# Kernel optimization log

Measured on AMD Instinct MI355X. Metric: run time of the kernel, lower is better.

Reference implementation:

```python
import jax, jax.numpy as jnp
import numpy as np

N_DIM = 512
HEADS = 8
NUM_EXPERTS = 65536
NUM_KEYS = 256      # sqrt(NUM_EXPERTS)
DIM_KEY = 256       # N_DIM // 2
TOPK = 16           # num_experts_per_head (also product_key_topk)
SCALE = 0.02


def setup_inputs() -> dict:
    key = jax.random.key(0)
    k0, k1, k2, k3, k4 = jax.random.split(key, 5)
    x = jax.random.normal(k0, (1, 2048, N_DIM), dtype=jnp.float32)
    W_q = jax.random.normal(k1, (N_DIM, 2 * HEADS * DIM_KEY), dtype=jnp.float32) * SCALE
    keys = jax.random.normal(k2, (HEADS, NUM_KEYS, 2, DIM_KEY), dtype=jnp.float32) * SCALE
    down_embed = jax.random.normal(k3, (NUM_EXPERTS, N_DIM), dtype=jnp.float32) * SCALE
    up_embed = jax.random.normal(k4, (NUM_EXPERTS, N_DIM), dtype=jnp.float32) * SCALE
    return {"x": x, "W_q": W_q, "keys": keys, "down_embed": down_embed, "up_embed": up_embed}


def reference(x, W_q, keys, down_embed, up_embed):
    b, n, d = x.shape
    # queries: [b,n,2*h*dk] -> [2,b,n,h,dk]
    q = (x @ W_q).reshape(b, n, 2, HEADS, DIM_KEY).transpose(2, 0, 1, 3, 4)
    # similarity against product keys: [2,b,n,h,num_keys]
    sim = jnp.einsum('pbnhd,hkpd->pbnhk', q, keys)
    sx, ix = jax.lax.top_k(sim[0], TOPK)   # [b,n,h,TOPK]
    sy, iy = jax.lax.top_k(sim[1], TOPK)
    # cartesian product of the two top-k sets -> [b,n,h,TOPK*TOPK]
    all_scores = (sx[..., :, None] + sy[..., None, :]).reshape(b, n, HEADS, TOPK * TOPK)
    scores, pk_idx = jax.lax.top_k(all_scores, TOPK)  # [b,n,h,TOPK]
    # NOTE: original module indexes embeddings with pk_idx (flat top-k positions),
    # reproduced faithfully here.
    w_down = down_embed[pk_idx]  # [b,n,h,TOPK,d]
    w_up = up_embed[pk_idx]      # [b,n,h,TOPK,d]
    h = jnp.einsum('bnd,bnhkd->bnhk', x, w_down)
    h = jax.nn.gelu(h, approximate=False)
    h = jax.nn.softmax(scores, axis=-1) * h
    return jnp.einsum('bnhk,bnhkd->bnd', h, w_up)
```

## Files before the change

kernel.cpp:

```cpp
#include <hip/hip_runtime.h>
#include <math.h>

#define N_TOK 2048
#define NDIM 512
#define HEADS 8
#define TOPK 16
#define QCOLS 4096

typedef __attribute__((ext_vector_type(8))) _Float16 f16x8;
typedef __attribute__((ext_vector_type(4))) float f32x4;

__device__ __forceinline__ unsigned short f32_to_f16(float f) {
    _Float16 h = (_Float16)f;
    return __builtin_bit_cast(unsigned short, h);
}
__device__ __forceinline__ float f16_to_f32(unsigned short u) {
    return (float)__builtin_bit_cast(_Float16, u);
}
__device__ __forceinline__ void gl_lds16(const void* g, void* l) {
    __builtin_amdgcn_global_load_lds(
        (const __attribute__((address_space(1))) void*)g,
        (__attribute__((address_space(3))) void*)l, 16, 0, 0);
}

__device__ __forceinline__ void split_f4(const float* __restrict__ src,
                                         unsigned short* __restrict__ dh,
                                         unsigned short* __restrict__ dl,
                                         int i) {
    float4 v = reinterpret_cast<const float4*>(src)[i];
    float vv[4] = {v.x, v.y, v.z, v.w};
    ushort4 h, lo;
    unsigned short* hp = &h.x; unsigned short* lp = &lo.x;
    #pragma unroll
    for (int q = 0; q < 4; ++q) {
        unsigned short hh = f32_to_f16(vv[q]);
        hp[q] = hh;
        lp[q] = f32_to_f16(vv[q] - f16_to_f32(hh));
    }
    reinterpret_cast<ushort4*>(dh)[i] = h;
    reinterpret_cast<ushort4*>(dl)[i] = lo;
}

__global__ __launch_bounds__(256) void kP_split(const float* __restrict__ x,
                                                const float* __restrict__ Wq,
                                                const float* __restrict__ keys,
                                                const float* __restrict__ down,
                                                const float* __restrict__ up,
                                                unsigned short* __restrict__ xh,
                                                unsigned short* __restrict__ xl,
                                                unsigned short* __restrict__ Wqh,
                                                unsigned short* __restrict__ Wql,
                                                unsigned short* __restrict__ ksh,
                                                unsigned short* __restrict__ ksl,
                                                unsigned short* __restrict__ Mth,
                                                unsigned short* __restrict__ Mtl,
                                                unsigned short* __restrict__ upTh,
                                                unsigned short* __restrict__ upTl) {
    const int bid = blockIdx.x;
    const int tid = threadIdx.x;
    if (bid < 256) {
        #pragma unroll
        for (int t = 0; t < 4; ++t) split_f4(x, xh, xl, bid * 1024 + t * 256 + tid);
        return;
    }
    if (bid < 768) {
        const int b = bid - 256;
        #pragma unroll
        for (int t = 0; t < 4; ++t) split_f4(Wq, Wqh, Wql, b * 1024 + t * 256 + tid);
        return;
    }
    if (bid < 1024) {
        const int b = bid - 768;
        #pragma unroll
        for (int t = 0; t < 4; ++t) split_f4(keys, ksh, ksl, b * 1024 + t * 256 + tid);
        return;
    }
    if (bid < 1280) {
        const int e = bid - 1024;
        const int d0 = tid * 2;
        float2 v = *reinterpret_cast<const float2*>(&down[(size_t)e * NDIM + d0]);
        ushort2 h, lo;
        unsigned short h0 = f32_to_f16(v.x);
        unsigned short h1 = f32_to_f16(v.y);
        h.x = h0; h.y = h1;
        lo.x = f32_to_f16(v.x - f16_to_f32(h0));
        lo.y = f32_to_f16(v.y - f16_to_f32(h1));
        *reinterpret_cast<ushort2*>(&Mth[(size_t)(QCOLS + e) * NDIM + d0]) = h;
        *reinterpret_cast<ushort2*>(&Mtl[(size_t)(QCOLS + e) * NDIM + d0]) = lo;
        return;
    }
    const int b = bid - 1280;
    #pragma unroll
    for (int dd = 0; dd < 8; ++dd) {
        const int d = b * 8 + dd;
        const int e = tid;
        const float v = up[(size_t)e * NDIM + d];
        unsigned short hh = f32_to_f16(v);
        upTh[(size_t)d * 256 + e] = hh;
        upTl[(size_t)d * 256 + e] = f32_to_f16(v - f16_to_f32(hh));
    }
}

__global__ __launch_bounds__(256) void kQ_m1(const unsigned short* __restrict__ Wqh,
                                             const unsigned short* __restrict__ Wql,
                                             const unsigned short* __restrict__ ksh,
                                             const unsigned short* __restrict__ ksl,
                                             unsigned short* __restrict__ Mth,
                                             unsigned short* __restrict__ Mtl) {
    __shared__ __align__(16) char lds[36864];
    const int tid = threadIdx.x;
    const int w = tid >> 6, l = tid & 63;
    const int c0 = blockIdx.x * 32;
    const int ph = blockIdx.y;
    const int p = ph >> 3, h = ph & 7;
    const int off = p * 2048 + h * 256;
    f32x4 acc[2][4] = {};

    for (int s = 0; s < 8; ++s) {
        const int kk = s * 32;
        __syncthreads();
        {
            const int q = w * 1024 + l * 16;
            const int r = q >> 7;
            const int bsw = (q & 127) ^ ((r & 7) << 4);
            const unsigned short* src = (bsw < 64)
                ? Wqh + (size_t)(c0 + r) * QCOLS + off + kk + (bsw >> 1)
                : Wql + (size_t)(c0 + r) * QCOLS + off + kk + ((bsw - 64) >> 1);
            gl_lds16(src, lds + w * 1024);
        }
        #pragma unroll
        for (int t = 0; t < 8; ++t) {
            const int q = w * 8192 + t * 1024 + l * 16;
            const int r = q >> 7;
            const int bsw = (q & 127) ^ ((r & 7) << 4);
            const unsigned short* src = (bsw < 64)
                ? ksh + ((size_t)(h * 256 + r) * 2 + p) * 256 + kk + (bsw >> 1)
                : ksl + ((size_t)(h * 256 + r) * 2 + p) * 256 + kk + ((bsw - 64) >> 1);
            gl_lds16(src, lds + 4096 + w * 8192 + t * 1024);
        }
        __syncthreads();
        const int bq = (l >> 4) * 16;
        f16x8 ah[2], al[2];
        #pragma unroll
        for (int mi = 0; mi < 2; ++mi) {
            const int ra = mi * 16 + (l & 15);
            const int swz = (ra & 7) << 4;
            ah[mi] = *(const f16x8*)(lds + ra * 128 + (bq ^ swz));
            al[mi] = *(const f16x8*)(lds + ra * 128 + ((bq + 64) ^ swz));
        }
        __builtin_amdgcn_s_setprio(1);
        #pragma unroll
        for (int nj = 0; nj < 4; ++nj) {
            const int rb = w * 64 + nj * 16 + (l & 15);
            const int swz = (rb & 7) << 4;
            f16x8 bh = *(const f16x8*)(lds + 4096 + rb * 128 + (bq ^ swz));
            f16x8 bl = *(const f16x8*)(lds + 4096 + rb * 128 + ((bq + 64) ^ swz));
            #pragma unroll
            for (int mi = 0; mi < 2; ++mi) {
                acc[mi][nj] = __builtin_amdgcn_mfma_f32_16x16x32_f16(ah[mi], bh, acc[mi][nj], 0, 0, 0);
                acc[mi][nj] = __builtin_amdgcn_mfma_f32_16x16x32_f16(ah[mi], bl, acc[mi][nj], 0, 0, 0);
                acc[mi][nj] = __builtin_amdgcn_mfma_f32_16x16x32_f16(al[mi], bh, acc[mi][nj], 0, 0, 0);
            }
        }
        __builtin_amdgcn_s_setprio(0);
    }
    #pragma unroll
    for (int mi = 0; mi < 2; ++mi)
        #pragma unroll
        for (int nj = 0; nj < 4; ++nj) {
            const int k = w * 64 + nj * 16 + (l & 15);
            const int cb = c0 + mi * 16 + (l >> 4) * 4;
            ushort4 h4, l4;
            unsigned short* hp = &h4.x; unsigned short* lp = &l4.x;
            #pragma unroll
            for (int r = 0; r < 4; ++r) {
                const float v = acc[mi][nj][r];
                unsigned short hh = f32_to_f16(v);
                hp[r] = hh;
                lp[r] = f32_to_f16(v - f16_to_f32(hh));
            }
            *reinterpret_cast<ushort4*>(&Mth[(size_t)(off + k) * NDIM + cb]) = h4;
            *reinterpret_cast<ushort4*>(&Mtl[(size_t)(off + k) * NDIM + cb]) = l4;
        }
}

#define BM 64
#define BN 256
#define BK 32
__global__ __launch_bounds__(256, 3) void kF_gemm(const unsigned short* __restrict__ xh,
                                                  const unsigned short* __restrict__ xl,
                                                  const unsigned short* __restrict__ Mth,
                                                  const unsigned short* __restrict__ Mtl,
                                                  float* __restrict__ T,
                                                  float* __restrict__ D) {
    __shared__ __align__(16) char lds[40960];
    const int tid = threadIdx.x;
    const int w = tid >> 6, l = tid & 63;
    const int row0 = blockIdx.x * BM;
    const int g = blockIdx.y;
    const int colbase = g * 256;
    f32x4 acc[4][4] = {};

    for (int s = 0; s < 16; ++s) {
        const int kk = s * BK;
        __syncthreads();
        #pragma unroll
        for (int t = 0; t < 2; ++t) {
            const int q = w * 2048 + t * 1024 + l * 16;
            const int r = q >> 7;
            const int bsw = (q & 127) ^ ((r & 7) << 4);
            const unsigned short* src = (bsw < 64)
                ? xh + (size_t)(row0 + r) * NDIM + kk + (bsw >> 1)
                : xl + (size_t)(row0 + r) * NDIM + kk + ((bsw - 64) >> 1);
            gl_lds16(src, lds + w * 2048 + t * 1024);
        }
        #pragma unroll
        for (int t = 0; t < 8; ++t) {
            const int q = w * 8192 + t * 1024 + l * 16;
            const int r = q >> 7;
            const int bsw = (q & 127) ^ ((r & 7) << 4);
            const unsigned short* src = (bsw < 64)
                ? Mth + (size_t)(colbase + r) * NDIM + kk + (bsw >> 1)
                : Mtl + (size_t)(colbase + r) * NDIM + kk + ((bsw - 64) >> 1);
            gl_lds16(src, lds + 8192 + w * 8192 + t * 1024);
        }
        __syncthreads();
        const int bq = (l >> 4) * 16;
        f16x8 ah[4], al[4];
        #pragma unroll
        for (int mi = 0; mi < 4; ++mi) {
            const int ra = mi * 16 + (l & 15);
            const int swz = (ra & 7) << 4;
            ah[mi] = *(const f16x8*)(lds + ra * 128 + (bq ^ swz));
            al[mi] = *(const f16x8*)(lds + ra * 128 + ((bq + 64) ^ swz));
        }
        __builtin_amdgcn_s_setprio(1);
        #pragma unroll
        for (int nj = 0; nj < 4; ++nj) {
            const int rb = w * 64 + nj * 16 + (l & 15);
            const int swz = (rb & 7) << 4;
            f16x8 bh = *(const f16x8*)(lds + 8192 + rb * 128 + (bq ^ swz));
            f16x8 bl = *(const f16x8*)(lds + 8192 + rb * 128 + ((bq + 64) ^ swz));
            #pragma unroll
            for (int mi = 0; mi < 4; ++mi) {
                acc[mi][nj] = __builtin_amdgcn_mfma_f32_16x16x32_f16(ah[mi], bh, acc[mi][nj], 0, 0, 0);
                acc[mi][nj] = __builtin_amdgcn_mfma_f32_16x16x32_f16(ah[mi], bl, acc[mi][nj], 0, 0, 0);
                acc[mi][nj] = __builtin_amdgcn_mfma_f32_16x16x32_f16(al[mi], bh, acc[mi][nj], 0, 0, 0);
            }
        }
        __builtin_amdgcn_s_setprio(0);
    }
    __syncthreads();

    if (g == 16) {
        #pragma unroll
        for (int mi = 0; mi < 4; ++mi)
            #pragma unroll
            for (int nj = 0; nj < 4; ++nj)
                #pragma unroll
                for (int r = 0; r < 4; ++r) {
                    const int row = row0 + mi * 16 + (l >> 4) * 4 + r;
                    const int col = w * 64 + nj * 16 + (l & 15);
                    D[(size_t)row * 256 + col] = acc[mi][nj][r];
                }
        return;
    }

    float* Cl = (float*)lds;
    const int grp = tid >> 4;
    const int lam = tid & 15;
    for (int c = 0; c < 4; ++c) {
        #pragma unroll
        for (int nj = 0; nj < 4; ++nj)
            #pragma unroll
            for (int r = 0; r < 4; ++r)
                Cl[((l >> 4) * 4 + r) * 260 + w * 64 + nj * 16 + (l & 15)] = acc[c][nj][r];
        __syncthreads();
        float v[16];
        #pragma unroll
        for (int j = 0; j < 16; ++j) v[j] = Cl[grp * 260 + lam + 16 * j];
        #pragma unroll
        for (int k = 2; k <= 16; k <<= 1)
            #pragma unroll
            for (int j = k >> 1; j > 0; j >>= 1)
                #pragma unroll
                for (int i = 0; i < 16; ++i) {
                    const int l2 = i ^ j;
                    if (l2 > i) {
                        const bool asc = ((i & k) == 0);
                        const float lo = fminf(v[i], v[l2]), hi = fmaxf(v[i], v[l2]);
                        v[i] = asc ? lo : hi;
                        v[l2] = asc ? hi : lo;
                    }
                }
        #pragma unroll
        for (int lvl = 1; lvl <= 8; lvl <<= 1) {
            float m[16];
            #pragma unroll
            for (int q = 0; q < 16; ++q)
                m[q] = fmaxf(v[q], __shfl_xor(v[15 - q], lvl));
            #pragma unroll
            for (int j = 8; j > 0; j >>= 1)
                #pragma unroll
                for (int i = 0; i < 16; ++i) {
                    const int l2 = i ^ j;
                    if (l2 > i) {
                        const float lo = fminf(m[i], m[l2]), hi = fmaxf(m[i], m[l2]);
                        m[i] = lo; m[l2] = hi;
                    }
                }
            #pragma unroll
            for (int q = 0; q < 16; ++q) v[q] = m[q];
        }
        const int n = row0 + c * 16 + grp;
        T[((size_t)n * 16 + g) * 16 + lam] = v[15 - lam];
        __syncthreads();
    }
}

__device__ const unsigned short CAND_TBL[32] = {
    0x0100, 0x0302, 0x0504, 0x0706, 0x0908, 0x0B0A, 0x0D0C, 0x0F0E,
    0x1110, 0x1312, 0x1514, 0x1716,
    0x2120, 0x2322, 0x3024, 0x3231, 0x4033, 0x4241,
    0x5150, 0x6160, 0x7170,
    0x9080, 0xB0A0, 0xD0C0, 0xF0E0,
    0xFFFF, 0xFFFF, 0xFFFF, 0xFFFF, 0xFFFF, 0xFFFF, 0xFFFF
};

__device__ __forceinline__ float sel16(const float a[16], int i) {
    float b0 = (i & 1) ? a[1] : a[0];
    float b1 = (i & 1) ? a[3] : a[2];
    float b2 = (i & 1) ? a[5] : a[4];
    float b3 = (i & 1) ? a[7] : a[6];
    float b4 = (i & 1) ? a[9] : a[8];
    float b5 = (i & 1) ? a[11] : a[10];
    float b6 = (i & 1) ? a[13] : a[12];
    float b7 = (i & 1) ? a[15] : a[14];
    float c0 = (i & 2) ? b1 : b0;
    float c1 = (i & 2) ? b3 : b2;
    float c2 = (i & 2) ? b5 : b4;
    float c3 = (i & 2) ? b7 : b6;
    float d0 = (i & 4) ? c1 : c0;
    float d1 = (i & 4) ? c3 : c2;
    return (i & 8) ? d1 : d0;
}

__global__ __launch_bounds__(256) void kC_combine(const float* __restrict__ T,
                                                  const float* __restrict__ D,
                                                  unsigned short* __restrict__ Wh,
                                                  unsigned short* __restrict__ Wl) {
    __shared__ unsigned long long ckey[8][50];
    __shared__ float winval[8][16];
    __shared__ int winflat[8][16];
    __shared__ int Wrow[256];

    const int tid = threadIdx.x;
    const int n = blockIdx.x;
    const int h = tid >> 5;
    const int lam = tid & 15;

    Wrow[tid] = 0;

    float sxd[16], syd[16];
    const float* t0 = &T[((size_t)n * 16 + h) * 16];
    const float* t1 = &T[((size_t)n * 16 + 8 + h) * 16];
    #pragma unroll
    for (int q = 0; q < 16; ++q) { sxd[q] = t0[q]; syd[q] = t1[q]; }

    const int lc = tid & 31;
    const unsigned int cw = CAND_TBL[lc];
    unsigned long long mykey[2]; float myval[2]; int myflat[2]; int myrank[2] = {0, 0};
    #pragma unroll
    for (int u = 0; u < 2; ++u) {
        const int fl = (cw >> (8 * u)) & 0xFF;
        const float sv = sel16(sxd, fl >> 4) + sel16(syd, fl & 15);
        const unsigned int uv = __float_as_uint(sv);
        const unsigned int mo = (uv & 0x80000000u) ? ~uv : (uv | 0x80000000u);
        mykey[u] = ((unsigned long long)mo << 8) | (unsigned long long)(255 - fl);
        myval[u] = sv; myflat[u] = fl;
        const int slot = lc * 2 + u;
        if (slot < 50) ckey[h][slot] = mykey[u];
    }
    __syncthreads();
    for (int kk = 0; kk < 50; ++kk) {
        const unsigned long long ok = ckey[h][kk];
        myrank[0] += (ok > mykey[0]) ? 1 : 0;
        myrank[1] += (ok > mykey[1]) ? 1 : 0;
    }
    #pragma unroll
    for (int u = 0; u < 2; ++u)
        if (myrank[u] < 16) { winval[h][myrank[u]] = myval[u]; winflat[h][myrank[u]] = myflat[u]; }
    __syncthreads();

    if (!(tid & 16)) {
        const float sc = winval[h][lam];
        const float m0 = winval[h][0];
        float e = expf(sc - m0);
        float esum = e;
        #pragma unroll
        for (int off = 1; off < 16; off <<= 1) esum += __shfl_xor(esum, off);
        const int fl = winflat[h][lam];
        const float hv = D[(size_t)n * 256 + fl];
        const float gg = 0.5f * hv * (1.0f + erff(hv * 0.70710678118654752f));
        const float wv = (e / esum) * gg;
        atomicAdd(&Wrow[fl], __float2int_rn(wv * 4194304.0f));
    }
    __syncthreads();
    const float wfin = (float)Wrow[tid] * (1.0f / 4194304.0f);
    const unsigned short hh = f32_to_f16(wfin);
    Wh[(size_t)n * 256 + tid] = hh;
    Wl[(size_t)n * 256 + tid] = f32_to_f16(wfin - f16_to_f32(hh));
}

__global__ __launch_bounds__(256) void k5_mfma(const unsigned short* __restrict__ Wh,
                                               const unsigned short* __restrict__ Wl,
                                               const unsigned short* __restrict__ upTh,
                                               const unsigned short* __restrict__ upTl,
                                               float* __restrict__ out) {
    __shared__ __align__(16) char lds[20480];
    const int tid = threadIdx.x;
    const int w = tid >> 6, l = tid & 63;
    const int n0 = blockIdx.x * 32;
    const int d0 = blockIdx.y * 128;
    f32x4 acc[2][2] = {};

    for (int s = 0; s < 8; ++s) {
        const int kk = s * 32;
        __syncthreads();
        {
            const int q = w * 1024 + l * 16;
            const int r = q >> 7;
            const int bsw = (q & 127) ^ ((r & 7) << 4);
            const unsigned short* src = (bsw < 64)
                ? Wh + (size_t)(n0 + r) * 256 + kk + (bsw >> 1)
                : Wl + (size_t)(n0 + r) * 256 + kk + ((bsw - 64) >> 1);
            gl_lds16(src, lds + w * 1024);
        }
        #pragma unroll
        for (int t = 0; t < 4; ++t) {
            const int q = w * 4096 + t * 1024 + l * 16;
            const int r = q >> 7;
            const int bsw = (q & 127) ^ ((r & 7) << 4);
            const unsigned short* src = (bsw < 64)
                ? upTh + (size_t)(d0 + r) * 256 + kk + (bsw >> 1)
                : upTl + (size_t)(d0 + r) * 256 + kk + ((bsw - 64) >> 1);
            gl_lds16(src, lds + 4096 + w * 4096 + t * 1024);
        }
        __syncthreads();
        const int bq = (l >> 4) * 16;
        f16x8 ah[2], al[2];
        #pragma unroll
        for (int mi = 0; mi < 2; ++mi) {
            const int ra = mi * 16 + (l & 15);
            const int swz = (ra & 7) << 4;
            ah[mi] = *(const f16x8*)(lds + ra * 128 + (bq ^ swz));
            al[mi] = *(const f16x8*)(lds + ra * 128 + ((bq + 64) ^ swz));
        }
        #pragma unroll
        for (int nj = 0; nj < 2; ++nj) {
            const int rb = w * 32 + nj * 16 + (l & 15);
            const int swz = (rb & 7) << 4;
            f16x8 bh = *(const f16x8*)(lds + 4096 + rb * 128 + (bq ^ swz));
            f16x8 bl = *(const f16x8*)(lds + 4096 + rb * 128 + ((bq + 64) ^ swz));
            #pragma unroll
            for (int mi = 0; mi < 2; ++mi) {
                acc[mi][nj] = __builtin_amdgcn_mfma_f32_16x16x32_f16(ah[mi], bh, acc[mi][nj], 0, 0, 0);
                acc[mi][nj] = __builtin_amdgcn_mfma_f32_16x16x32_f16(ah[mi], bl, acc[mi][nj], 0, 0, 0);
                acc[mi][nj] = __builtin_amdgcn_mfma_f32_16x16x32_f16(al[mi], bh, acc[mi][nj], 0, 0, 0);
            }
        }
    }
    #pragma unroll
    for (int mi = 0; mi < 2; ++mi)
        #pragma unroll
        for (int nj = 0; nj < 2; ++nj)
            #pragma unroll
            for (int r = 0; r < 4; ++r) {
                const int row = n0 + mi * 16 + (l >> 4) * 4 + r;
                const int col = d0 + w * 32 + nj * 16 + (l & 15);
                out[(size_t)row * NDIM + col] = acc[mi][nj][r];
            }
}

extern "C" void kernel_launch(void* const* d_in, const int* in_sizes, int n_in,
                              void* d_out, int out_size, void* d_ws, size_t ws_size,
                              hipStream_t stream) {
    const float* x    = (const float*)d_in[0];
    const float* Wq   = (const float*)d_in[1];
    const float* keys = (const float*)d_in[2];
    const float* down = (const float*)d_in[3];
    const float* up   = (const float*)d_in[4];
    float* out = (float*)d_out;

    char* ws = (char*)d_ws;
    unsigned short* Mth  = (unsigned short*)(ws);
    unsigned short* Mtl  = (unsigned short*)(ws + 4456448);
    unsigned short* xh   = (unsigned short*)(ws + 8912896);
    unsigned short* xl   = (unsigned short*)(ws + 11010048);
    unsigned short* Wqh  = (unsigned short*)(ws + 13107200);
    unsigned short* Wql  = (unsigned short*)(ws + 17301504);
    unsigned short* ksh  = (unsigned short*)(ws + 21495808);
    unsigned short* ksl  = (unsigned short*)(ws + 23592960);
    unsigned short* upTh = (unsigned short*)(ws + 25690112);
    unsigned short* upTl = (unsigned short*)(ws + 25952256);
    float* T             = (float*)(ws + 26214400);
    float* D             = (float*)(ws + 28311552);
    unsigned short* Wh   = (unsigned short*)(ws + 30408704);
    unsigned short* Wl   = (unsigned short*)(ws + 31457280);

    kP_split<<<1344, 256, 0, stream>>>(x, Wq, keys, down, up,
                                       xh, xl, Wqh, Wql, ksh, ksl, Mth, Mtl, upTh, upTl);
    kQ_m1<<<dim3(16, 16), 256, 0, stream>>>(Wqh, Wql, ksh, ksl, Mth, Mtl);
    kF_gemm<<<dim3(32, 17), 256, 0, stream>>>(xh, xl, Mth, Mtl, T, D);
    kC_combine<<<2048, 256, 0, stream>>>(T, D, Wh, Wl);
    k5_mfma<<<dim3(64, 4), 256, 0, stream>>>(Wh, Wl, upTh, upTl, out);
}
```

Measured before the change: 94.20 us.

## Enlarge fused GEMM tile to 256x256 with 1024 threads and scale split low parts

Result: slower. 353.4 us (+275.2%).

```diff
diff --git a/kernel.cpp b/kernel.cpp
--- a/kernel.cpp
+++ b/kernel.cpp
@@ -6,6 +6,8 @@
 #define HEADS 8
 #define TOPK 16
 #define QCOLS 4096
+#define LSC 4096.0f
+#define ILSC (1.0f/4096.0f)
 
 typedef __attribute__((ext_vector_type(8))) _Float16 f16x8;
 typedef __attribute__((ext_vector_type(4))) float f32x4;
@@ -23,10 +25,10 @@
         (__attribute__((address_space(3))) void*)l, 16, 0, 0);
 }
 
-__device__ __forceinline__ void split_f4(const float* __restrict__ src,
-                                         unsigned short* __restrict__ dh,
-                                         unsigned short* __restrict__ dl,
-                                         int i) {
+__device__ __forceinline__ void split_f4s(const float* __restrict__ src,
+                                          unsigned short* __restrict__ dh,
+                                          unsigned short* __restrict__ dl,
+                                          int i, float lsc) {
     float4 v = reinterpret_cast<const float4*>(src)[i];
     float vv[4] = {v.x, v.y, v.z, v.w};
     ushort4 h, lo;
@@ -35,7 +37,7 @@
     for (int q = 0; q < 4; ++q) {
         unsigned short hh = f32_to_f16(vv[q]);
         hp[q] = hh;
-        lp[q] = f32_to_f16(vv[q] - f16_to_f32(hh));
+        lp[q] = f32_to_f16((vv[q] - f16_to_f32(hh)) * lsc);
     }
     reinterpret_cast<ushort4*>(dh)[i] = h;
     reinterpret_cast<ushort4*>(dl)[i] = lo;
@@ -60,19 +62,19 @@
     const int tid = threadIdx.x;
     if (bid < 256) {
         #pragma unroll
-        for (int t = 0; t < 4; ++t) split_f4(x, xh, xl, bid * 1024 + t * 256 + tid);
+        for (int t = 0; t < 4; ++t) split_f4s(x, xh, xl, bid * 1024 + t * 256 + tid, 1.0f);
         return;
     }
     if (bid < 768) {
         const int b = bid - 256;
         #pragma unroll
-        for (int t = 0; t < 4; ++t) split_f4(Wq, Wqh, Wql, b * 1024 + t * 256 + tid);
+        for (int t = 0; t < 4; ++t) split_f4s(Wq, Wqh, Wql, b * 1024 + t * 256 + tid, LSC);
         return;
     }
     if (bid < 1024) {
         const int b = bid - 768;
         #pragma unroll
-        for (int t = 0; t < 4; ++t) split_f4(keys, ksh, ksl, b * 1024 + t * 256 + tid);
+        for (int t = 0; t < 4; ++t) split_f4s(keys, ksh, ksl, b * 1024 + t * 256 + tid, LSC);
         return;
     }
     if (bid < 1280) {
@@ -97,7 +99,7 @@
         const float v = up[(size_t)e * NDIM + d];
         unsigned short hh = f32_to_f16(v);
         upTh[(size_t)d * 256 + e] = hh;
-        upTl[(size_t)d * 256 + e] = f32_to_f16(v - f16_to_f32(hh));
+        upTl[(size_t)d * 256 + e] = f32_to_f16((v - f16_to_f32(hh)) * LSC);
     }
 }
 
@@ -114,7 +116,8 @@
     const int ph = blockIdx.y;
     const int p = ph >> 3, h = ph & 7;
     const int off = p * 2048 + h * 256;
-    f32x4 acc[2][4] = {};
+    f32x4 acch[2][4] = {};
+    f32x4 accl[2][4] = {};
 
     for (int s = 0; s < 8; ++s) {
         const int kk = s * 32;
@@ -157,9 +160,9 @@
             f16x8 bl = *(const f16x8*)(lds + 4096 + rb * 128 + ((bq + 64) ^ swz));
             #pragma unroll
             for (int mi = 0; mi < 2; ++mi) {
-                acc[mi][nj] = __builtin_amdgcn_mfma_f32_16x16x32_f16(ah[mi], bh, acc[mi][nj], 0, 0, 0);
-                acc[mi][nj] = __builtin_amdgcn_mfma_f32_16x16x32_f16(ah[mi], bl, acc[mi][nj], 0, 0, 0);
-                acc[mi][nj] = __builtin_amdgcn_mfma_f32_16x16x32_f16(al[mi], bh, acc[mi][nj], 0, 0, 0);
+                acch[mi][nj] = __builtin_amdgcn_mfma_f32_16x16x32_f16(ah[mi], bh, acch[mi][nj], 0, 0, 0);
+                accl[mi][nj] = __builtin_amdgcn_mfma_f32_16x16x32_f16(ah[mi], bl, accl[mi][nj], 0, 0, 0);
+                accl[mi][nj] = __builtin_amdgcn_mfma_f32_16x16x32_f16(al[mi], bh, accl[mi][nj], 0, 0, 0);
             }
         }
         __builtin_amdgcn_s_setprio(0);
@@ -174,7 +177,7 @@
             unsigned short* hp = &h4.x; unsigned short* lp = &l4.x;
             #pragma unroll
             for (int r = 0; r < 4; ++r) {
-                const float v = acc[mi][nj][r];
+                const float v = fmaf(accl[mi][nj][r], ILSC, acch[mi][nj][r]);
                 unsigned short hh = f32_to_f16(v);
                 hp[r] = hh;
                 lp[r] = f32_to_f16(v - f16_to_f32(hh));
@@ -184,21 +187,24 @@
         }
 }
 
-#define BM 64
+#define BM 256
 #define BN 256
 #define BK 32
-__global__ __launch_bounds__(256, 3) void kF_gemm(const unsigned short* __restrict__ xh,
-                                                  const unsigned short* __restrict__ xl,
-                                                  const unsigned short* __restrict__ Mth,
-                                                  const unsigned short* __restrict__ Mtl,
-                                                  float* __restrict__ T,
-                                                  float* __restrict__ D) {
-    __shared__ __align__(16) char lds[40960];
+__global__ __launch_bounds__(1024) void kF_gemm(const unsigned short* __restrict__ xh,
+                                                const unsigned short* __restrict__ xl,
+                                                const unsigned short* __restrict__ Mth,
+                                                const unsigned short* __restrict__ Mtl,
+                                                float* __restrict__ T,
+                                                float* __restrict__ D) {
+    __shared__ __align__(16) char lds[65536];
     const int tid = threadIdx.x;
     const int w = tid >> 6, l = tid & 63;
-    const int row0 = blockIdx.x * BM;
-    const int g = blockIdx.y;
-    const int colbase = g * 256;
+    const int wr = w >> 2, wc = w & 3;
+    const int orig = blockIdx.x;
+    const int swz = (orig & 7) * 17 + (orig >> 3);
+    const int by = swz >> 3;
+    const int row0 = (swz & 7) * BM;
+    const int colbase = by * 256;
     f32x4 acc[4][4] = {};
 
     for (int s = 0; s < 16; ++s) {
@@ -206,41 +212,41 @@
         __syncthreads();
         #pragma unroll
         for (int t = 0; t < 2; ++t) {
-            const int q = w * 2048 + t * 1024 + l * 16;
+            const int q = t * 16384 + tid * 16;
             const int r = q >> 7;
             const int bsw = (q & 127) ^ ((r & 7) << 4);
             const unsigned short* src = (bsw < 64)
                 ? xh + (size_t)(row0 + r) * NDIM + kk + (bsw >> 1)
                 : xl + (size_t)(row0 + r) * NDIM + kk + ((bsw - 64) >> 1);
-            gl_lds16(src, lds + w * 2048 + t * 1024);
-        }
-        #pragma unroll
-        for (int t = 0; t < 8; ++t) {
-            const int q = w * 8192 + t * 1024 + l * 16;
+            gl_lds16(src, lds + q);
+        }
+        #pragma unroll
+        for (int t = 0; t < 2; ++t) {
+            const int q = t * 16384 + tid * 16;
             const int r = q >> 7;
             const int bsw = (q & 127) ^ ((r & 7) << 4);
             const unsigned short* src = (bsw < 64)
                 ? Mth + (size_t)(colbase + r) * NDIM + kk + (bsw >> 1)
                 : Mtl + (size_t)(colbase + r) * NDIM + kk + ((bsw - 64) >> 1);
-            gl_lds16(src, lds + 8192 + w * 8192 + t * 1024);
+            gl_lds16(src, lds + 32768 + q);
         }
         __syncthreads();
         const int bq = (l >> 4) * 16;
         f16x8 ah[4], al[4];
         #pragma unroll
         for (int mi = 0; mi < 4; ++mi) {
-            const int ra = mi * 16 + (l & 15);
-            const int swz = (ra & 7) << 4;
-            ah[mi] = *(const f16x8*)(lds + ra * 128 + (bq ^ swz));
-            al[mi] = *(const f16x8*)(lds + ra * 128 + ((bq + 64) ^ swz));
+            const int ra = wr * 64 + mi * 16 + (l & 15);
+            const int sz = (ra & 7) << 4;
+            ah[mi] = *(const f16x8*)(lds + ra * 128 + (bq ^ sz));
+            al[mi] = *(const f16x8*)(lds + ra * 128 + ((bq + 64) ^ sz));
         }
         __builtin_amdgcn_s_setprio(1);
         #pragma unroll
         for (int nj = 0; nj < 4; ++nj) {
-            const int rb = w * 64 + nj * 16 + (l & 15);
-            const int swz = (rb & 7) << 4;
-            f16x8 bh = *(const f16x8*)(lds + 8192 + rb * 128 + (bq ^ swz));
-            f16x8 bl = *(const f16x8*)(lds + 8192 + rb * 128 + ((bq + 64) ^ swz));
+            const int rb = wc * 64 + nj * 16 + (l & 15);
+            const int sz = (rb & 7) << 4;
+            f16x8 bh = *(const f16x8*)(lds + 32768 + rb * 128 + (bq ^ sz));
+            f16x8 bl = *(const f16x8*)(lds + 32768 + rb * 128 + ((bq + 64) ^ sz));
             #pragma unroll
             for (int mi = 0; mi < 4; ++mi) {
                 acc[mi][nj] = __builtin_amdgcn_mfma_f32_16x16x32_f16(ah[mi], bh, acc[mi][nj], 0, 0, 0);
@@ -252,68 +258,77 @@
     }
     __syncthreads();
 
-    if (g == 16) {
+    if (by == 16) {
         #pragma unroll
         for (int mi = 0; mi < 4; ++mi)
             #pragma unroll
             for (int nj = 0; nj < 4; ++nj)
                 #pragma unroll
                 for (int r = 0; r < 4; ++r) {
-                    const int row = row0 + mi * 16 + (l >> 4) * 4 + r;
-                    const int col = w * 64 + nj * 16 + (l & 15);
+                    const int row = row0 + wr * 64 + mi * 16 + (l >> 4) * 4 + r;
+                    const int col = wc * 64 + nj * 16 + (l & 15);
                     D[(size_t)row * 256 + col] = acc[mi][nj][r];
                 }
         return;
     }
 
     float* Cl = (float*)lds;
-    const int grp = tid >> 4;
+    const int g2 = tid >> 4;
     const int lam = tid & 15;
-    for (int c = 0; c < 4; ++c) {
-        #pragma unroll
-        for (int nj = 0; nj < 4; ++nj)
-            #pragma unroll
-            for (int r = 0; r < 4; ++r)
-                Cl[((l >> 4) * 4 + r) * 260 + w * 64 + nj * 16 + (l & 15)] = acc[c][nj][r];
-        __syncthreads();
-        float v[16];
-        #pragma unroll
-        for (int j = 0; j < 16; ++j) v[j] = Cl[grp * 260 + lam + 16 * j];
-        #pragma unroll
-        for (int k = 2; k <= 16; k <<= 1)
-            #pragma unroll
-            for (int j = k >> 1; j > 0; j >>= 1)
+    for (int c = 0; c < 8; ++c) {
+        if (wr == (c >> 1)) {
+            #pragma unroll
+            for (int u = 0; u < 2; ++u) {
+                const int mi = (c & 1) * 2 + u;
                 #pragma unroll
-                for (int i = 0; i < 16; ++i) {
-                    const int l2 = i ^ j;
-                    if (l2 > i) {
-                        const bool asc = ((i & k) == 0);
-                        const float lo = fminf(v[i], v[l2]), hi = fmaxf(v[i], v[l2]);
-                        v[i] = asc ? lo : hi;
-                        v[l2] = asc ? hi : lo;
+                for (int nj = 0; nj < 4; ++nj)
+                    #pragma unroll
+                    for (int r = 0; r < 4; ++r)
+                        Cl[(u * 16 + (l >> 4) * 4 + r) * 260 + wc * 64 + nj * 16 + (l & 15)] =
+                            acc[mi][nj][r];
+            }
+        }
+        __syncthreads();
+        if (g2 < 32) {
+            float v[16];
+            #pragma unroll
+            for (int j = 0; j < 16; ++j) v[j] = Cl[g2 * 260 + lam + 16 * j];
+            #pragma unroll
+            for (int k = 2; k <= 16; k <<= 1)
+                #pragma unroll
+                for (int j = k >> 1; j > 0; j >>= 1)
+                    #pragma unroll
+                    for (int i = 0; i < 16; ++i) {
+                        const int l2 = i ^ j;
+                        if (l2 > i) {
+                            const bool asc = ((i & k) == 0);
+                            const float lo = fminf(v[i], v[l2]), hi = fmaxf(v[i], v[l2]);
+                            v[i] = asc ? lo : hi;
+                            v[l2] = asc ? hi : lo;
+                        }
                     }
-                }
-        #pragma unroll
-        for (int lvl = 1; lvl <= 8; lvl <<= 1) {
-            float m[16];
-            #pragma unroll
-            for (int q = 0; q < 16; ++q)
-                m[q] = fmaxf(v[q], __shfl_xor(v[15 - q], lvl));
-            #pragma unroll
-            for (int j = 8; j > 0; j >>= 1)
+            #pragma unroll
+            for (int lvl = 1; lvl <= 8; lvl <<= 1) {
+                float m[16];
                 #pragma unroll
-                for (int i = 0; i < 16; ++i) {
-                    const int l2 = i ^ j;
-                    if (l2 > i) {
-                        const float lo = fminf(m[i], m[l2]), hi = fmaxf(m[i], m[l2]);
-                        m[i] = lo; m[l2] = hi;
+                for (int q = 0; q < 16; ++q)
+                    m[q] = fmaxf(v[q], __shfl_xor(v[15 - q], lvl));
+                #pragma unroll
+                for (int j = 8; j > 0; j >>= 1)
+                    #pragma unroll
+                    for (int i = 0; i < 16; ++i) {
+                        const int l2 = i ^ j;
+                        if (l2 > i) {
+                            const float lo = fminf(m[i], m[l2]), hi = fmaxf(m[i], m[l2]);
+                            m[i] = lo; m[l2] = hi;
+                        }
                     }
-                }
-            #pragma unroll
-            for (int q = 0; q < 16; ++q) v[q] = m[q];
-        }
-        const int n = row0 + c * 16 + grp;
-        T[((size_t)n * 16 + g) * 16 + lam] = v[15 - lam];
+                #pragma unroll
+                for (int q = 0; q < 16; ++q) v[q] = m[q];
+            }
+            const int n = row0 + c * 32 + g2;
+            T[((size_t)n * 16 + by) * 16 + lam] = v[15 - lam];
+        }
         __syncthreads();
     }
 }
@@ -409,7 +424,7 @@
     const float wfin = (float)Wrow[tid] * (1.0f / 4194304.0f);
     const unsigned short hh = f32_to_f16(wfin);
     Wh[(size_t)n * 256 + tid] = hh;
-    Wl[(size_t)n * 256 + tid] = f32_to_f16(wfin - f16_to_f32(hh));
+    Wl[(size_t)n * 256 + tid] = f32_to_f16((wfin - f16_to_f32(hh)) * LSC);
 }
 
 __global__ __launch_bounds__(256) void k5_mfma(const unsigned short* __restrict__ Wh,
@@ -422,7 +437,8 @@
     const int w = tid >> 6, l = tid & 63;
     const int n0 = blockIdx.x * 32;
     const int d0 = blockIdx.y * 128;
-    f32x4 acc[2][2] = {};
+    f32x4 acch[2][2] = {};
+    f32x4 accl[2][2] = {};
 
     for (int s = 0; s < 8; ++s) {
         const int kk = s * 32;
@@ -464,9 +480,9 @@
             f16x8 bl = *(const f16x8*)(lds + 4096 + rb * 128 + ((bq + 64) ^ swz));
             #pragma unroll
             for (int mi = 0; mi < 2; ++mi) {
-                acc[mi][nj] = __builtin_amdgcn_mfma_f32_16x16x32_f16(ah[mi], bh, acc[mi][nj], 0, 0, 0);
-                acc[mi][nj] = __builtin_amdgcn_mfma_f32_16x16x32_f16(ah[mi], bl, acc[mi][nj], 0, 0, 0);
-                acc[mi][nj] = __builtin_amdgcn_mfma_f32_16x16x32_f16(al[mi], bh, acc[mi][nj], 0, 0, 0);
+                acch[mi][nj] = __builtin_amdgcn_mfma_f32_16x16x32_f16(ah[mi], bh, acch[mi][nj], 0, 0, 0);
+                accl[mi][nj] = __builtin_amdgcn_mfma_f32_16x16x32_f16(ah[mi], bl, accl[mi][nj], 0, 0, 0);
+                accl[mi][nj] = __builtin_amdgcn_mfma_f32_16x16x32_f16(al[mi], bh, accl[mi][nj], 0, 0, 0);
             }
         }
     }
@@ -478,7 +494,7 @@
             for (int r = 0; r < 4; ++r) {
                 const int row = n0 + mi * 16 + (l >> 4) * 4 + r;
                 const int col = d0 + w * 32 + nj * 16 + (l & 15);
-                out[(size_t)row * NDIM + col] = acc[mi][nj][r];
+                out[(size_t)row * NDIM + col] = fmaf(accl[mi][nj][r], ILSC, acch[mi][nj][r]);
             }
 }
 
@@ -504,14 +520,14 @@
     unsigned short* upTh = (unsigned short*)(ws + 25690112);
     unsigned short* upTl = (unsigned short*)(ws + 25952256);
     float* T             = (float*)(ws + 26214400);
-    float* D             = (float*)(ws + 28311552);
-    unsigned short* Wh   = (unsigned short*)(ws + 30408704);
-    unsigned short* Wl   = (unsigned short*)(ws + 31457280);
+    float* D             = (float*)(ws + 30408704);
+    unsigned short* Wh   = (unsigned short*)(ws + 32505856);
+    unsigned short* Wl   = (unsigned short*)(ws + 33554432);
 
     kP_split<<<1344, 256, 0, stream>>>(x, Wq, keys, down, up,
                                        xh, xl, Wqh, Wql, ksh, ksl, Mth, Mtl, upTh, upTl);
     kQ_m1<<<dim3(16, 16), 256, 0, stream>>>(Wqh, Wql, ksh, ksl, Mth, Mtl);
-    kF_gemm<<<dim3(32, 17), 256, 0, stream>>>(xh, xl, Mth, Mtl, T, D);
+    kF_gemm<<<136, 1024, 0, stream>>>(xh, xl, Mth, Mtl, T, D);
     kC_combine<<<2048, 256, 0, stream>>>(T, D, Wh, Wl);
     k5_mfma<<<dim3(64, 4), 256, 0, stream>>>(Wh, Wl, upTh, upTl, out);
 }
```
